# Performance work log

Hardware: AMD Instinct MI355X
Metric: run time of the kernel (lower is better)

Reference implementation:

```python
import jax, jax.numpy as jnp
import numpy as np

N_NODES = 50000
N_EDGES = 800000
D_FEAT = 64


def setup_inputs() -> dict:
    key = jax.random.key(0)
    kx, ks, kd = jax.random.split(key, 3)
    x = jax.random.normal(kx, (N_NODES, D_FEAT), dtype=jnp.float32)
    src = jax.random.randint(ks, (N_EDGES,), 0, N_NODES, dtype=jnp.int64)
    dst = jax.random.randint(kd, (N_EDGES,), 0, N_NODES, dtype=jnp.int64)
    return {"x": x, "src": src, "dst": dst}


def reference(x, src, dst):
    # SGC propagation: h[v] = sum_{(u->v) in E} x[u] / sqrt(out_deg(u) * out_deg(v))
    n = x.shape[0]
    # out-degrees: count of outgoing edges per node (matches graph.out_degrees())
    deg = jax.ops.segment_sum(jnp.ones(src.shape, x.dtype), src, num_segments=n)
    # per-edge normalization coefficient 1/sqrt(deg_u * deg_v)  [E]
    norm = 1.0 / jnp.sqrt(deg[src] * deg[dst])
    # gather-multiply-scatter-sum (u_mul_e_sum): messages flow src -> dst
    h = jax.ops.segment_sum(x[src] * norm[:, None], dst, num_segments=n)
    return h
```

## Files before the change

### kernel.cpp

```cpp
#include <hip/hip_runtime.h>

#define N_NODES 50000
#define N_EDGES 800000
#define D_FEAT 64

#define NBINS 2048
#define BSORT 100
#define SORT_CHUNK (N_EDGES / BSORT)
#define NSCAN (NBINS * BSORT)
#define SCAN_BLOCK 1024
#define SCAN_BLOCKS (NSCAN / SCAN_BLOCK)
#define AGG_CAP 4096
#define NAGG ((N_NODES + 31) / 32)

#define HCHUNKS 64
#define HCHUNK (N_EDGES / HCHUNKS)
#define HWORDS ((N_NODES + 3) / 4)

__global__ __launch_bounds__(256)
void hist_outdeg_kernel(const int* __restrict__ src, unsigned int* __restrict__ hp32) {
    __shared__ unsigned int lh[HWORDS];
    const int chunk = blockIdx.x;
    const int t = threadIdx.x;
    for (int i = t; i < HWORDS; i += 256) lh[i] = 0u;
    __syncthreads();
    const int4* s4 = (const int4*)(src + chunk * HCHUNK);
    for (int i = t; i < HCHUNK / 4; i += 256) {
        int4 v = s4[i];
        atomicAdd(&lh[v.x >> 2], 1u << ((v.x & 3) * 8));
        atomicAdd(&lh[v.y >> 2], 1u << ((v.y & 3) * 8));
        atomicAdd(&lh[v.z >> 2], 1u << ((v.z & 3) * 8));
        atomicAdd(&lh[v.w >> 2], 1u << ((v.w & 3) * 8));
    }
    __syncthreads();
    for (int w = t; w < HWORDS; w += 256)
        hp32[(size_t)chunk * HWORDS + w] = lh[w];
}

__global__ __launch_bounds__(256)
void count_rs_kernel(const int* __restrict__ dst, unsigned int* __restrict__ gh,
                     const unsigned char* __restrict__ hp8, float* __restrict__ rs) {
    __shared__ unsigned int lh[NBINS];
    const int b = blockIdx.x, t = threadIdx.x;
    if (b < BSORT) {
        for (int i = t; i < NBINS; i += 256) lh[i] = 0;
        __syncthreads();
        const int4* d4 = (const int4*)(dst + b * SORT_CHUNK);
        for (int i = t; i < SORT_CHUNK / 4; i += 256) {
            int4 v = d4[i];
            atomicAdd(&lh[v.x >> 5], 1u);
            atomicAdd(&lh[v.y >> 5], 1u);
            atomicAdd(&lh[v.z >> 5], 1u);
            atomicAdd(&lh[v.w >> 5], 1u);
        }
        __syncthreads();
        for (int i = t; i < NBINS; i += 256) gh[(size_t)i * BSORT + b] = lh[i];
    } else {
        int v = (b - BSORT) * 256 + t;
        if (v < N_NODES) {
            unsigned int s = 0;
            #pragma unroll
            for (int c = 0; c < HCHUNKS; ++c) s += hp8[(size_t)c * (HWORDS * 4) + v];
            rs[v] = rsqrtf((float)s);
        }
    }
}

__global__ __launch_bounds__(SCAN_BLOCK)
void scan_reduce_kernel(const unsigned int* __restrict__ in, unsigned int* __restrict__ partial) {
    __shared__ unsigned int wsum[SCAN_BLOCK / 64];
    int g = blockIdx.x * SCAN_BLOCK + threadIdx.x;
    unsigned int v = in[g];
    for (int off = 32; off > 0; off >>= 1) v += __shfl_down(v, off, 64);
    if ((threadIdx.x & 63) == 0) wsum[threadIdx.x >> 6] = v;
    __syncthreads();
    if (threadIdx.x < SCAN_BLOCK / 64) {
        unsigned int s = wsum[threadIdx.x];
        for (int off = SCAN_BLOCK / 128; off > 0; off >>= 1) s += __shfl_down(s, off, 64);
        if (threadIdx.x == 0) partial[blockIdx.x] = s;
    }
}

__global__ __launch_bounds__(SCAN_BLOCK)
void scan_final_kernel(unsigned int* __restrict__ data, const unsigned int* __restrict__ partial) {
    __shared__ unsigned int arr[SCAN_BLOCK];
    __shared__ unsigned int pbase[256];
    const int t = threadIdx.x;
    const int g = blockIdx.x * SCAN_BLOCK + t;
    if (t < 256) pbase[t] = (t < SCAN_BLOCKS) ? partial[t] : 0u;
    __syncthreads();
    for (int off = 1; off < 256; off <<= 1) {
        unsigned int u = (t < 256 && t >= off) ? pbase[t - off] : 0u;
        __syncthreads();
        if (t < 256 && t >= off) pbase[t] += u;
        __syncthreads();
    }
    const unsigned int base = (blockIdx.x == 0) ? 0u : pbase[blockIdx.x - 1];
    unsigned int v = data[g];
    arr[t] = v;
    __syncthreads();
    for (int off = 1; off < SCAN_BLOCK; off <<= 1) {
        unsigned int u = (t >= off) ? arr[t - off] : 0u;
        __syncthreads();
        arr[t] += u;
        __syncthreads();
    }
    data[g] = base + arr[t] - v;
}

__global__ __launch_bounds__(256)
void bucket_scatter_kernel(const int* __restrict__ src, const int* __restrict__ dst,
                           const unsigned int* __restrict__ gh, unsigned int* __restrict__ keysB) {
    __shared__ unsigned int cur[NBINS];
    const int b = blockIdx.x, t = threadIdx.x;
    for (int i = t; i < NBINS; i += 256) cur[i] = gh[(size_t)i * BSORT + b];
    __syncthreads();
    const int4* s4 = (const int4*)(src + b * SORT_CHUNK);
    const int4* d4 = (const int4*)(dst + b * SORT_CHUNK);
    for (int i = t; i < SORT_CHUNK / 4; i += 256) {
        int4 s = s4[i];
        int4 d = d4[i];
        unsigned int p0 = atomicAdd(&cur[d.x >> 5], 1u);
        keysB[p0] = ((unsigned int)d.x << 16) | (unsigned int)s.x;
        unsigned int p1 = atomicAdd(&cur[d.y >> 5], 1u);
        keysB[p1] = ((unsigned int)d.y << 16) | (unsigned int)s.y;
        unsigned int p2 = atomicAdd(&cur[d.z >> 5], 1u);
        keysB[p2] = ((unsigned int)d.z << 16) | (unsigned int)s.z;
        unsigned int p3 = atomicAdd(&cur[d.w >> 5], 1u);
        keysB[p3] = ((unsigned int)d.w << 16) | (unsigned int)s.w;
    }
}

__global__ __launch_bounds__(256)
void bucket_aggregate_kernel(const float* __restrict__ x, const unsigned int* __restrict__ gh,
                             const unsigned int* __restrict__ keysB, const float* __restrict__ rs,
                             float* __restrict__ h) {
    __shared__ unsigned int ebuf[AGG_CAP];
    __shared__ unsigned int ecnt[32];
    __shared__ unsigned int eoff[33];
    const int g = blockIdx.x;
    const int t = threadIdx.x;
    const int lane = t & 63;
    const int w = t >> 6;
    const unsigned int base = gh[(size_t)g * BSORT];
    const unsigned int end  = gh[(size_t)(g + 1) * BSORT];
    const int cnt = (int)(end - base);

    if (cnt > 0 && cnt <= AGG_CAP) {
        if (t < 32) ecnt[t] = 0;
        __syncthreads();
        for (int i = t; i < cnt; i += 256) {
            unsigned int k = keysB[base + i];
            atomicAdd(&ecnt[(k >> 16) & 31], 1u);
        }
        __syncthreads();
        if (t == 0) {
            unsigned int r = 0;
            for (int k2 = 0; k2 < 32; ++k2) { eoff[k2] = r; r += ecnt[k2]; }
            eoff[32] = r;
        }
        __syncthreads();
        if (t < 32) ecnt[t] = eoff[t];
        __syncthreads();
        for (int i = t; i < cnt; i += 256) {
            unsigned int k = keysB[base + i];
            unsigned int p = atomicAdd(&ecnt[(k >> 16) & 31], 1u);
            ebuf[p] = k;
        }
        __syncthreads();
        for (int nl = w; nl < 32; nl += 4) {
            int node = g * 32 + nl;
            if (node >= N_NODES) continue;
            int jb = (int)eoff[nl], je = (int)eoff[nl + 1];
            float acc = 0.0f;
            int j = jb;
            for (; j + 3 < je; j += 4) {
                unsigned int k0 = ebuf[j], k1 = ebuf[j + 1], k2 = ebuf[j + 2], k3 = ebuf[j + 3];
                unsigned int s0 = k0 & 0xFFFFu, s1 = k1 & 0xFFFFu;
                unsigned int s2 = k2 & 0xFFFFu, s3 = k3 & 0xFFFFu;
                float w0 = rs[s0], w1 = rs[s1], w2 = rs[s2], w3 = rs[s3];
                acc = fmaf(x[(size_t)s0 * D_FEAT + lane], w0, acc);
                acc = fmaf(x[(size_t)s1 * D_FEAT + lane], w1, acc);
                acc = fmaf(x[(size_t)s2 * D_FEAT + lane], w2, acc);
                acc = fmaf(x[(size_t)s3 * D_FEAT + lane], w3, acc);
            }
            for (; j < je; ++j) {
                unsigned int k = ebuf[j];
                unsigned int s = k & 0xFFFFu;
                acc = fmaf(x[(size_t)s * D_FEAT + lane], rs[s], acc);
            }
            h[(size_t)node * D_FEAT + lane] = (je > jb) ? acc * rs[node] : 0.0f;
        }
    } else {
        for (int nl = w; nl < 32; nl += 4) {
            int node = g * 32 + nl;
            if (node >= N_NODES) continue;
            float acc = 0.0f;
            int any = 0;
            for (unsigned int j = base; j < end; ++j) {
                unsigned int k = keysB[j];
                if ((int)((k >> 16) & 31) == nl) {
                    unsigned int s = k & 0xFFFFu;
                    acc = fmaf(x[(size_t)s * D_FEAT + lane], rs[s], acc);
                    any = 1;
                }
            }
            h[(size_t)node * D_FEAT + lane] = any ? acc * rs[node] : 0.0f;
        }
    }
}

__global__ void fb_degree_kernel(const int* __restrict__ src, unsigned int* __restrict__ deg,
                                 int n_edges) {
    int i = blockIdx.x * blockDim.x + threadIdx.x;
    int stride = gridDim.x * blockDim.x;
    for (; i < n_edges; i += stride) atomicAdd(&deg[src[i]], 1u);
}
__global__ void fb_scatter_kernel(const float* __restrict__ x, const int* __restrict__ src,
                                  const int* __restrict__ dst, const unsigned int* __restrict__ deg,
                                  float* __restrict__ h, int n_edges) {
    const int lane = threadIdx.x & 63;
    const int wave = (int)((blockIdx.x * blockDim.x + threadIdx.x) >> 6);
    const int nwaves = (int)((gridDim.x * blockDim.x) >> 6);
    for (int e = wave; e < n_edges; e += nwaves) {
        int s = __builtin_amdgcn_readfirstlane(src[e]);
        int d = __builtin_amdgcn_readfirstlane(dst[e]);
        float norm = rsqrtf((float)deg[s] * (float)deg[d]);
        atomicAdd(&h[d * D_FEAT + lane], x[s * D_FEAT + lane] * norm);
    }
}

extern "C" void kernel_launch(void* const* d_in, const int* in_sizes, int n_in,
                              void* d_out, int out_size, void* d_ws, size_t ws_size,
                              hipStream_t stream) {
    const float* x   = (const float*)d_in[0];
    const int*   src = (const int*)d_in[1];
    const int*   dst = (const int*)d_in[2];
    float* h = (float*)d_out;

    size_t off = 0;
    unsigned int*  keysB = (unsigned int*)((char*)d_ws + off);  off += (size_t)N_EDGES * 4;
    unsigned int*  hp32  = keysB;
    unsigned int*  gh    = (unsigned int*)((char*)d_ws + off);  off += (size_t)NSCAN * 4;
    float*         rs    = (float*)((char*)d_ws + off);         off += (size_t)N_NODES * 4;
    unsigned int*  spart = (unsigned int*)((char*)d_ws + off);  off += 256 * 4;

    if (ws_size >= off) {
        hist_outdeg_kernel<<<dim3(HCHUNKS), dim3(256), 0, stream>>>(src, hp32);
        count_rs_kernel<<<dim3(BSORT + (N_NODES + 255) / 256), dim3(256), 0, stream>>>(
            dst, gh, (const unsigned char*)hp32, rs);
        scan_reduce_kernel<<<dim3(SCAN_BLOCKS), dim3(SCAN_BLOCK), 0, stream>>>(gh, spart);
        scan_final_kernel<<<dim3(SCAN_BLOCKS), dim3(SCAN_BLOCK), 0, stream>>>(gh, spart);
        bucket_scatter_kernel<<<dim3(BSORT), dim3(256), 0, stream>>>(src, dst, gh, keysB);
        bucket_aggregate_kernel<<<dim3(NAGG), dim3(256), 0, stream>>>(x, gh, keysB, rs, h);
    } else {
        unsigned int* deg = (unsigned int*)d_ws;
        hipMemsetAsync(deg, 0, N_NODES * sizeof(unsigned int), stream);
        hipMemsetAsync(d_out, 0, (size_t)out_size * sizeof(float), stream);
        fb_degree_kernel<<<dim3(1024), dim3(256), 0, stream>>>(src, deg, N_EDGES);
        fb_scatter_kernel<<<dim3(2048), dim3(256), 0, stream>>>(x, src, dst, deg, h, N_EDGES);
    }
}
```

Baseline: 69.28 us.

## Prescale source features and store as bf16 for aggregation gathers

Fuses the out-degree normalization of each source node into a preprocessing pass, which writes x*rsqrt(deg) as a bf16 copy in workspace. The aggregation kernel then gathers 2-byte values with no per-edge rs lookup. This halves gather traffic and removes the random rs reads. The cost is an extra full pass over x and reduced precision in the accumulated inputs.

Measured after the change: 84.25 us. +21.6%, slower.

```diff
diff --git a/kernel.cpp b/kernel.cpp
--- a/kernel.cpp
+++ b/kernel.cpp
@@ -1,4 +1,5 @@
 #include <hip/hip_runtime.h>
+#include <hip/hip_bf16.h>
 
 #define N_NODES 50000
 #define N_EDGES 800000
@@ -17,6 +18,8 @@
 #define HCHUNK (N_EDGES / HCHUNKS)
 #define HWORDS ((N_NODES + 3) / 4)
 
+#define CONV_BLOCKS ((N_NODES + 255) / 256)
+
 __global__ __launch_bounds__(256)
 void hist_outdeg_kernel(const int* __restrict__ src, unsigned int* __restrict__ hp32) {
     __shared__ unsigned int lh[HWORDS];
@@ -38,9 +41,11 @@
 }
 
 __global__ __launch_bounds__(256)
-void count_rs_kernel(const int* __restrict__ dst, unsigned int* __restrict__ gh,
-                     const unsigned char* __restrict__ hp8, float* __restrict__ rs) {
+void count_rs_conv_kernel(const int* __restrict__ dst, unsigned int* __restrict__ gh,
+                          const unsigned char* __restrict__ hp8, float* __restrict__ rs,
+                          const float* __restrict__ x, unsigned short* __restrict__ xb) {
     __shared__ unsigned int lh[NBINS];
+    __shared__ float lrs[256];
     const int b = blockIdx.x, t = threadIdx.x;
     if (b < BSORT) {
         for (int i = t; i < NBINS; i += 256) lh[i] = 0;
@@ -56,12 +61,30 @@
         __syncthreads();
         for (int i = t; i < NBINS; i += 256) gh[(size_t)i * BSORT + b] = lh[i];
     } else {
-        int v = (b - BSORT) * 256 + t;
+        const int nb = (b - BSORT) * 256;
+        const int v = nb + t;
+        float w = 0.0f;
         if (v < N_NODES) {
             unsigned int s = 0;
             #pragma unroll
             for (int c = 0; c < HCHUNKS; ++c) s += hp8[(size_t)c * (HWORDS * 4) + v];
-            rs[v] = rsqrtf((float)s);
+            w = rsqrtf((float)s);
+            rs[v] = w;
+        }
+        if (xb != nullptr) {
+            lrs[t] = w;
+            __syncthreads();
+            #pragma unroll 4
+            for (int it = 0; it < 64; ++it) {
+                int idx = it * 256 + t;
+                int nl = idx >> 6;
+                int g = nb + nl;
+                if (g < N_NODES) {
+                    float f = x[(size_t)g * D_FEAT + (idx & 63)] * lrs[nl];
+                    xb[(size_t)g * D_FEAT + (idx & 63)] =
+                        __hip_bfloat16_raw(__float2bfloat16(f)).x;
+                }
+            }
         }
     }
 }
@@ -132,6 +155,80 @@
 }
 
 __global__ __launch_bounds__(256)
+void bucket_aggregate_bf16_kernel(const unsigned short* __restrict__ xb,
+                                  const unsigned int* __restrict__ gh,
+                                  const unsigned int* __restrict__ keysB,
+                                  const float* __restrict__ rs, float* __restrict__ h) {
+    __shared__ unsigned int ebuf[AGG_CAP];
+    __shared__ unsigned int ecnt[32];
+    __shared__ unsigned int eoff[33];
+    const int g = blockIdx.x;
+    const int t = threadIdx.x;
+    const int lane = t & 63;
+    const int w = t >> 6;
+    const unsigned int base = gh[(size_t)g * BSORT];
+    const unsigned int end  = gh[(size_t)(g + 1) * BSORT];
+    const int cnt = (int)(end - base);
+
+    if (cnt > 0 && cnt <= AGG_CAP) {
+        if (t < 32) ecnt[t] = 0;
+        __syncthreads();
+        for (int i = t; i < cnt; i += 256) atomicAdd(&ecnt[(keysB[base + i] >> 16) & 31], 1u);
+        __syncthreads();
+        if (t == 0) {
+            unsigned int r = 0;
+            for (int k2 = 0; k2 < 32; ++k2) { eoff[k2] = r; r += ecnt[k2]; }
+            eoff[32] = r;
+        }
+        __syncthreads();
+        if (t < 32) ecnt[t] = eoff[t];
+        __syncthreads();
+        for (int i = t; i < cnt; i += 256) {
+            unsigned int k = keysB[base + i];
+            ebuf[atomicAdd(&ecnt[(k >> 16) & 31], 1u)] = k;
+        }
+        __syncthreads();
+        for (int nl = w; nl < 32; nl += 4) {
+            int node = g * 32 + nl;
+            if (node >= N_NODES) continue;
+            int jb = (int)eoff[nl], je = (int)eoff[nl + 1];
+            float acc = 0.0f;
+            int j = jb;
+            for (; j + 3 < je; j += 4) {
+                unsigned int s0 = ebuf[j] & 0xFFFFu,     s1 = ebuf[j + 1] & 0xFFFFu;
+                unsigned int s2 = ebuf[j + 2] & 0xFFFFu, s3 = ebuf[j + 3] & 0xFFFFu;
+                unsigned int v0 = xb[(size_t)s0 * D_FEAT + lane];
+                unsigned int v1 = xb[(size_t)s1 * D_FEAT + lane];
+                unsigned int v2 = xb[(size_t)s2 * D_FEAT + lane];
+                unsigned int v3 = xb[(size_t)s3 * D_FEAT + lane];
+                acc += __uint_as_float(v0 << 16) + __uint_as_float(v1 << 16);
+                acc += __uint_as_float(v2 << 16) + __uint_as_float(v3 << 16);
+            }
+            for (; j < je; ++j) {
+                unsigned int s = ebuf[j] & 0xFFFFu;
+                acc += __uint_as_float((unsigned int)xb[(size_t)s * D_FEAT + lane] << 16);
+            }
+            h[(size_t)node * D_FEAT + lane] = (je > jb) ? acc * rs[node] : 0.0f;
+        }
+    } else {
+        for (int nl = w; nl < 32; nl += 4) {
+            int node = g * 32 + nl;
+            if (node >= N_NODES) continue;
+            float acc = 0.0f;
+            int any = 0;
+            for (unsigned int j = base; j < end; ++j) {
+                unsigned int k = keysB[j];
+                if ((int)((k >> 16) & 31) == nl) {
+                    acc += __uint_as_float((unsigned int)xb[(size_t)(k & 0xFFFFu) * D_FEAT + lane] << 16);
+                    any = 1;
+                }
+            }
+            h[(size_t)node * D_FEAT + lane] = any ? acc * rs[node] : 0.0f;
+        }
+    }
+}
+
+__global__ __launch_bounds__(256)
 void bucket_aggregate_kernel(const float* __restrict__ x, const unsigned int* __restrict__ gh,
                              const unsigned int* __restrict__ keysB, const float* __restrict__ rs,
                              float* __restrict__ h) {
@@ -149,10 +246,7 @@
     if (cnt > 0 && cnt <= AGG_CAP) {
         if (t < 32) ecnt[t] = 0;
         __syncthreads();
-        for (int i = t; i < cnt; i += 256) {
-            unsigned int k = keysB[base + i];
-            atomicAdd(&ecnt[(k >> 16) & 31], 1u);
-        }
+        for (int i = t; i < cnt; i += 256) atomicAdd(&ecnt[(keysB[base + i] >> 16) & 31], 1u);
         __syncthreads();
         if (t == 0) {
             unsigned int r = 0;
@@ -164,8 +258,7 @@
         __syncthreads();
         for (int i = t; i < cnt; i += 256) {
             unsigned int k = keysB[base + i];
-            unsigned int p = atomicAdd(&ecnt[(k >> 16) & 31], 1u);
-            ebuf[p] = k;
+            ebuf[atomicAdd(&ecnt[(k >> 16) & 31], 1u)] = k;
         }
         __syncthreads();
         for (int nl = w; nl < 32; nl += 4) {
@@ -175,9 +268,8 @@
             float acc = 0.0f;
             int j = jb;
             for (; j + 3 < je; j += 4) {
-                unsigned int k0 = ebuf[j], k1 = ebuf[j + 1], k2 = ebuf[j + 2], k3 = ebuf[j + 3];
-                unsigned int s0 = k0 & 0xFFFFu, s1 = k1 & 0xFFFFu;
-                unsigned int s2 = k2 & 0xFFFFu, s3 = k3 & 0xFFFFu;
+                unsigned int s0 = ebuf[j] & 0xFFFFu,     s1 = ebuf[j + 1] & 0xFFFFu;
+                unsigned int s2 = ebuf[j + 2] & 0xFFFFu, s3 = ebuf[j + 3] & 0xFFFFu;
                 float w0 = rs[s0], w1 = rs[s1], w2 = rs[s2], w3 = rs[s3];
                 acc = fmaf(x[(size_t)s0 * D_FEAT + lane], w0, acc);
                 acc = fmaf(x[(size_t)s1 * D_FEAT + lane], w1, acc);
@@ -185,8 +277,7 @@
                 acc = fmaf(x[(size_t)s3 * D_FEAT + lane], w3, acc);
             }
             for (; j < je; ++j) {
-                unsigned int k = ebuf[j];
-                unsigned int s = k & 0xFFFFu;
+                unsigned int s = ebuf[j] & 0xFFFFu;
                 acc = fmaf(x[(size_t)s * D_FEAT + lane], rs[s], acc);
             }
             h[(size_t)node * D_FEAT + lane] = (je > jb) ? acc * rs[node] : 0.0f;
@@ -244,15 +335,23 @@
     unsigned int*  gh    = (unsigned int*)((char*)d_ws + off);  off += (size_t)NSCAN * 4;
     float*         rs    = (float*)((char*)d_ws + off);         off += (size_t)N_NODES * 4;
     unsigned int*  spart = (unsigned int*)((char*)d_ws + off);  off += 256 * 4;
-
-    if (ws_size >= off) {
+    const size_t off_b = off;
+    unsigned short* xb  = (unsigned short*)((char*)d_ws + off); off += (size_t)N_NODES * D_FEAT * 2;
+    const size_t off_a = off;
+
+    if (ws_size >= off_b) {
+        const bool tierA = (ws_size >= off_a);
         hist_outdeg_kernel<<<dim3(HCHUNKS), dim3(256), 0, stream>>>(src, hp32);
-        count_rs_kernel<<<dim3(BSORT + (N_NODES + 255) / 256), dim3(256), 0, stream>>>(
-            dst, gh, (const unsigned char*)hp32, rs);
+        count_rs_conv_kernel<<<dim3(BSORT + CONV_BLOCKS), dim3(256), 0, stream>>>(
+            dst, gh, (const unsigned char*)hp32, rs, x, tierA ? xb : nullptr);
         scan_reduce_kernel<<<dim3(SCAN_BLOCKS), dim3(SCAN_BLOCK), 0, stream>>>(gh, spart);
         scan_final_kernel<<<dim3(SCAN_BLOCKS), dim3(SCAN_BLOCK), 0, stream>>>(gh, spart);
         bucket_scatter_kernel<<<dim3(BSORT), dim3(256), 0, stream>>>(src, dst, gh, keysB);
-        bucket_aggregate_kernel<<<dim3(NAGG), dim3(256), 0, stream>>>(x, gh, keysB, rs, h);
+        if (tierA) {
+            bucket_aggregate_bf16_kernel<<<dim3(NAGG), dim3(256), 0, stream>>>(xb, gh, keysB, rs, h);
+        } else {
+            bucket_aggregate_kernel<<<dim3(NAGG), dim3(256), 0, stream>>>(x, gh, keysB, rs, h);
+        }
     } else {
         unsigned int* deg = (unsigned int*)d_ws;
         hipMemsetAsync(deg, 0, N_NODES * sizeof(unsigned int), stream);
```
